# Performance work log

Hardware: AMD Instinct MI355X
Metric: run time of the kernel (lower is better)

## Reference

```python
import jax, jax.numpy as jnp
import numpy as np

TEMP = 0.1        # ds_temperature
THRESHOLD = 0.2
MARGIN = 2        # margin_remove


def setup_inputs() -> dict:
    key = jax.random.key(0)
    k0, k1 = jax.random.split(key)
    N, C = 2, 256
    h0, w0, h1, w1 = 60, 80, 60, 80
    feature0 = jax.random.normal(k0, (N, h0 * w0, C), dtype=jnp.float32)
    feature1 = jax.random.normal(k1, (N, h1 * w1, C), dtype=jnp.float32)
    return {"feature0": feature0, "feature1": feature1,
            "h0": h0, "w0": w0, "h1": h1, "w1": w1}


def _interior(n: int, b: int) -> jnp.ndarray:
    # True on [b, n-b), mirroring mask[:, :b]=False and mask[:, -b:]=False
    a = jnp.arange(n)
    return (a >= b) & (a < n - b)


def reference(feature0, feature1, h0, w0, h1, w1):
    N, L, C = feature0.shape
    S = feature1.shape[1]
    # similarities: (f0/sqrt(C)) . (f1/sqrt(C)) / temp == f0.f1 / (C*temp)
    sim = jnp.einsum('nlc,nsc->nls', feature0, feature1) / (C * TEMP)
    # dual softmax confidences
    conf = jax.nn.softmax(sim, axis=2) * jax.nn.softmax(sim, axis=1)
    # threshold mask with spatial margin removal (mask0 is None branch)
    mask = conf > THRESHOLD                      # [N, L, S]
    m5 = mask.reshape(N, h0, w0, h1, w1)
    valid = (_interior(h0, MARGIN)[:, None, None, None]
             & _interior(w0, MARGIN)[None, :, None, None]
             & _interior(h1, MARGIN)[None, None, :, None]
             & _interior(w1, MARGIN)[None, None, None, :])
    m5 = m5 & valid[None]
    mask = m5.reshape(N, L, S)
    # mutual nearest neighbor constraint
    mutual = ((conf == conf.max(axis=2, keepdims=True))
              & (conf == conf.max(axis=1, keepdims=True)))
    mask = mask & mutual
    # dense (jit-safe) encoding of the matches: confidences zeroed off-match.
    matched_conf = jnp.where(mask, conf, 0.0)
    return conf, mask, matched_conf
```

## Files before the change

kernel.cpp:

```cpp
#include <hip/hip_runtime.h>

#define NB 2
#define LD 4800
#define SD 4800
#define CD 256
#define H0 60
#define W0 80
#define H1 60
#define W1 80
#define MG 2
#define THRESH 0.2f
#define SIM_SCALE (1.0f / (256.0f * 0.1f))
#define GT 38
#define CAP 8192

typedef float f32x4 __attribute__((ext_vector_type(4)));
typedef __bf16 bf16x8 __attribute__((ext_vector_type(8)));
typedef unsigned short u16x8 __attribute__((ext_vector_type(8)));

#define GLOBAL_AS __attribute__((address_space(1)))
#define LDS_AS __attribute__((address_space(3)))

__device__ __forceinline__ void gl_lds16(const unsigned short* g, unsigned short* l) {
    __builtin_amdgcn_global_load_lds((const GLOBAL_AS unsigned int*)g,
                                     (LDS_AS unsigned int*)l, 16, 0, 0);
}

__device__ __forceinline__ unsigned short f2bf(float f) {
    unsigned int u = __float_as_uint(f);
    u = u + 0x7FFFu + ((u >> 16) & 1u);
    return (unsigned short)(u >> 16);
}

__device__ __forceinline__ bool interior0(int idx) {
    int i = idx / W0, j = idx % W0;
    return (i >= MG) & (i < H0 - MG) & (j >= MG) & (j < W0 - MG);
}
__device__ __forceinline__ bool interior1(int idx) {
    int i = idx / W1, j = idx % W1;
    return (i >= MG) & (i < H1 - MG) & (j >= MG) & (j < W1 - MG);
}

__global__ __launch_bounds__(256) void k_prep(float* __restrict__ p, int n) {
    int i = blockIdx.x * 256 + threadIdx.x;
    if (i < n) p[i] = 0.f;
}

__global__ __launch_bounds__(256) void k_cvt(const float* __restrict__ src,
                                             unsigned short* __restrict__ dst, int n8) {
    int i = blockIdx.x * 256 + threadIdx.x;
    if (i >= n8) return;
    const float4* s = (const float4*)src + (size_t)i * 2;
    float4 a = s[0], b = s[1];
    u16x8 o = {f2bf(a.x), f2bf(a.y), f2bf(a.z), f2bf(a.w),
               f2bf(b.x), f2bf(b.y), f2bf(b.z), f2bf(b.w)};
    *(u16x8*)(dst + (size_t)i * 8) = o;
}

template <int PASS>
__global__ __launch_bounds__(256) void k_gemm(const unsigned short* __restrict__ bA,
                                              const unsigned short* __restrict__ bB,
                                              float* __restrict__ rowsum,
                                              float* __restrict__ colsum,
                                              float* __restrict__ conf,
                                              float* __restrict__ mask,
                                              unsigned int* __restrict__ rowmax,
                                              unsigned int* __restrict__ colmax,
                                              unsigned int* __restrict__ cnt,
                                              uint4* __restrict__ list) {
    __shared__ __align__(16) unsigned short As[128][32];
    __shared__ __align__(16) unsigned short Bs[128][32];

    const int n  = blockIdx.z;
    const int s0 = blockIdx.x * 128;
    const int l0 = blockIdx.y * 128;
    const int tid  = threadIdx.x;
    const int lane = tid & 63;
    const int wave = tid >> 6;
    const int wm = (wave >> 1) * 64;
    const int wn = (wave & 1) * 64;
    const int quad = lane >> 4;
    const int lr   = lane & 15;

    const int sr = wave * 32 + (lane >> 2);
    const int sc = (lane & 3) * 8;
    const unsigned short* ga0 = bA + ((size_t)n * LD + min(l0 + sr,      LD - 1)) * CD + sc;
    const unsigned short* ga1 = bA + ((size_t)n * LD + min(l0 + sr + 16, LD - 1)) * CD + sc;
    const unsigned short* gb0 = bB + ((size_t)n * SD + min(s0 + sr,      SD - 1)) * CD + sc;
    const unsigned short* gb1 = bB + ((size_t)n * SD + min(s0 + sr + 16, SD - 1)) * CD + sc;
    unsigned short* la0 = &As[wave * 32][0];
    unsigned short* la1 = &As[wave * 32 + 16][0];
    unsigned short* lb0 = &Bs[wave * 32][0];
    unsigned short* lb1 = &Bs[wave * 32 + 16][0];

    f32x4 acc[4][4];
#pragma unroll
    for (int i = 0; i < 4; ++i)
#pragma unroll
        for (int j = 0; j < 4; ++j) acc[i][j] = (f32x4){0.f, 0.f, 0.f, 0.f};

    for (int k0 = 0; k0 < CD; k0 += 32) {
        __syncthreads();
        gl_lds16(ga0 + k0, la0);
        gl_lds16(ga1 + k0, la1);
        gl_lds16(gb0 + k0, lb0);
        gl_lds16(gb1 + k0, lb1);
        __syncthreads();

        bf16x8 af[4], bfr[4];
#pragma unroll
        for (int i = 0; i < 4; ++i) {
            af[i]  = __builtin_bit_cast(bf16x8, *(const u16x8*)&As[wm + i * 16 + lr][quad * 8]);
            bfr[i] = __builtin_bit_cast(bf16x8, *(const u16x8*)&Bs[wn + i * 16 + lr][quad * 8]);
        }
#pragma unroll
        for (int i = 0; i < 4; ++i)
#pragma unroll
            for (int j = 0; j < 4; ++j)
                acc[i][j] = __builtin_amdgcn_mfma_f32_16x16x32_bf16(af[i], bfr[j], acc[i][j], 0, 0, 0);
    }

    const int rb = l0 + wm;
    const int cb = s0 + wn;

    if (PASS == 0) {
        float rpart[4][4];
        float cpart[4];
#pragma unroll
        for (int i = 0; i < 4; ++i) {
            cpart[i] = 0.f;
#pragma unroll
            for (int g = 0; g < 4; ++g) rpart[i][g] = 0.f;
        }
#pragma unroll
        for (int mi = 0; mi < 4; ++mi)
#pragma unroll
            for (int ni = 0; ni < 4; ++ni)
#pragma unroll
                for (int g = 0; g < 4; ++g) {
                    int row = rb + mi * 16 + quad * 4 + g;
                    int col = cb + ni * 16 + lr;
                    float sv = acc[mi][ni][g] * SIM_SCALE;
                    bool ok = (row < LD) & (col < SD);
                    float ev = ok ? __expf(sv) : 0.f;
                    rpart[mi][g] += ev;
                    cpart[ni] += ev;
                }
#pragma unroll
        for (int mi = 0; mi < 4; ++mi)
#pragma unroll
            for (int g = 0; g < 4; ++g) {
                float v = rpart[mi][g];
                v += __shfl_xor(v, 1);
                v += __shfl_xor(v, 2);
                v += __shfl_xor(v, 4);
                v += __shfl_xor(v, 8);
                int row = rb + mi * 16 + quad * 4 + g;
                if (lr == 0 && row < LD) atomicAdd(&rowsum[n * LD + row], v);
            }
#pragma unroll
        for (int ni = 0; ni < 4; ++ni) {
            float v = cpart[ni];
            v += __shfl_xor(v, 16);
            v += __shfl_xor(v, 32);
            int col = cb + ni * 16 + lr;
            if (quad == 0 && col < SD) atomicAdd(&colsum[n * SD + col], v);
        }
    } else {
        {
            const size_t plane = (size_t)NB * LD * SD;
            f32x4* mask4  = (f32x4*)mask;
            f32x4* match4 = (f32x4*)(mask + plane);
            const int r0 = tid >> 5;
            const int c4 = tid & 31;
            const f32x4 z = {0.f, 0.f, 0.f, 0.f};
            if (s0 + c4 * 4 < SD) {
#pragma unroll
                for (int rr = 0; rr < 16; ++rr) {
                    int row = l0 + r0 + rr * 8;
                    if (row < LD) {
                        size_t o = ((size_t)n * LD + row) * (SD / 4) + (s0 / 4) + c4;
                        mask4[o]  = z;
                        match4[o] = z;
                    }
                }
            }
        }

        float rinv[4][4], cinv[4];
#pragma unroll
        for (int mi = 0; mi < 4; ++mi)
#pragma unroll
            for (int g = 0; g < 4; ++g) {
                int row = min(rb + mi * 16 + quad * 4 + g, LD - 1);
                rinv[mi][g] = rowsum[n * LD + row];
            }
#pragma unroll
        for (int ni = 0; ni < 4; ++ni) {
            int col = min(cb + ni * 16 + lr, SD - 1);
            cinv[ni] = colsum[n * SD + col];
        }
#pragma unroll
        for (int mi = 0; mi < 4; ++mi)
#pragma unroll
            for (int ni = 0; ni < 4; ++ni)
#pragma unroll
                for (int g = 0; g < 4; ++g) {
                    int row = rb + mi * 16 + quad * 4 + g;
                    int col = cb + ni * 16 + lr;
                    float sv = acc[mi][ni][g] * SIM_SCALE;
                    float e = __expf(sv);
                    float cv = e * e * rinv[mi][g] * cinv[ni];
                    bool ok = (row < LD) & (col < SD);
                    if (ok) {
                        conf[((size_t)n * LD + row) * SD + col] = cv;
                        if (cv > THRESH) {
                            atomicMax(&rowmax[n * LD + row], __float_as_uint(cv));
                            atomicMax(&colmax[n * SD + col], __float_as_uint(cv));
                            unsigned int id = atomicAdd(cnt, 1u);
                            if (id < CAP) {
                                uint4 rec = {(unsigned)n, (unsigned)row, (unsigned)col,
                                             __float_as_uint(cv)};
                                list[id] = rec;
                            }
                        }
                    }
                }
    }
}

__global__ __launch_bounds__(256) void k_inv(float* __restrict__ p, int n) {
    int i = blockIdx.x * 256 + threadIdx.x;
    if (i < n) p[i] = 1.0f / p[i];
}

__global__ __launch_bounds__(256) void k_fix(const unsigned int* __restrict__ cnt,
                                             const uint4* __restrict__ list,
                                             const unsigned int* __restrict__ rowmax,
                                             const unsigned int* __restrict__ colmax,
                                             float* __restrict__ mask,
                                             float* __restrict__ matched) {
    unsigned int m = min(*cnt, (unsigned int)CAP);
    for (unsigned int i = threadIdx.x; i < m; i += 256) {
        uint4 r = list[i];
        int n = (int)r.x, row = (int)r.y, col = (int)r.z;
        unsigned int cb = r.w;
        if (cb == rowmax[n * LD + row] && cb == colmax[n * SD + col] &&
            interior0(row) && interior1(col)) {
            size_t o = ((size_t)n * LD + row) * SD + col;
            mask[o] = 1.f;
            matched[o] = __uint_as_float(cb);
        }
    }
}

extern "C" void kernel_launch(void* const* d_in, const int* in_sizes, int n_in,
                              void* d_out, int out_size, void* d_ws, size_t ws_size,
                              hipStream_t stream) {
    const float* f0 = (const float*)d_in[0];
    const float* f1 = (const float*)d_in[1];
    const size_t plane = (size_t)NB * LD * SD;
    float* conf = (float*)d_out;
    float* mask = conf + plane;

    float* rowsum = (float*)d_ws;
    float* colsum = rowsum + NB * LD;
    unsigned int* rowmaxu = (unsigned int*)(colsum + NB * SD);
    unsigned int* colmaxu = rowmaxu + NB * LD;
    unsigned int* cnt = colmaxu + NB * SD;
    uint4* list = (uint4*)(cnt + 4);
    unsigned short* bf0 = (unsigned short*)(list + CAP);
    unsigned short* bf1 = bf0 + (size_t)NB * LD * CD;

    const int nz = NB * (LD + SD) * 2 + 4;
    k_prep<<<dim3((nz + 255) / 256), 256, 0, stream>>>(rowsum, nz);
    const int n8 = NB * LD * CD / 8;
    k_cvt<<<dim3((n8 + 255) / 256), 256, 0, stream>>>(f0, bf0, n8);
    k_cvt<<<dim3((n8 + 255) / 256), 256, 0, stream>>>(f1, bf1, n8);

    dim3 gg(GT, GT, NB);
    k_gemm<0><<<gg, 256, 0, stream>>>(bf0, bf1, rowsum, colsum, nullptr, nullptr,
                                      nullptr, nullptr, nullptr, nullptr);
    const int ninv = NB * (LD + SD);
    k_inv<<<dim3((ninv + 255) / 256), 256, 0, stream>>>(rowsum, ninv);
    k_gemm<1><<<gg, 256, 0, stream>>>(bf0, bf1, rowsum, colsum, conf, mask,
                                      rowmaxu, colmaxu, cnt, list);
    k_fix<<<dim3(1), 256, 0, stream>>>(cnt, list, rowmaxu, colmaxu, mask, mask + plane);
}
```

Baseline: 669.6 us.

## Stage conf epilogue through LDS for coalesced stores, double-buffer K loop, fuse prep kernels

The pass-1 epilogue now writes normalized confidences into an LDS buffer and stores them back as coalesced float4 rows, replacing scattered per-element global stores. The GEMM K loop is double-buffered so the next tile loads while the current one is multiplied. The zero-init and the two bf16 convert kernels are merged into one launch, and the reciprocal kernel is folded into the epilogue. This costs more LDS (a union of the tiles and a 64x132 float buffer) and an extra sync round per half-tile, which may lower occupancy.

```diff
diff --git a/kernel.cpp b/kernel.cpp
--- a/kernel.cpp
+++ b/kernel.cpp
@@ -41,21 +41,32 @@
     return (i >= MG) & (i < H1 - MG) & (j >= MG) & (j < W1 - MG);
 }
 
-__global__ __launch_bounds__(256) void k_prep(float* __restrict__ p, int n) {
-    int i = blockIdx.x * 256 + threadIdx.x;
-    if (i < n) p[i] = 0.f;
-}
-
-__global__ __launch_bounds__(256) void k_cvt(const float* __restrict__ src,
-                                             unsigned short* __restrict__ dst, int n8) {
-    int i = blockIdx.x * 256 + threadIdx.x;
-    if (i >= n8) return;
-    const float4* s = (const float4*)src + (size_t)i * 2;
-    float4 a = s[0], b = s[1];
-    u16x8 o = {f2bf(a.x), f2bf(a.y), f2bf(a.z), f2bf(a.w),
-               f2bf(b.x), f2bf(b.y), f2bf(b.z), f2bf(b.w)};
-    *(u16x8*)(dst + (size_t)i * 8) = o;
-}
+__global__ __launch_bounds__(256) void k_init(const float* __restrict__ f0,
+                                              const float* __restrict__ f1,
+                                              unsigned short* __restrict__ bf0,
+                                              unsigned short* __restrict__ bf1,
+                                              float* __restrict__ stats, int nstat) {
+    const int per = NB * LD * CD / 8;
+    int t = blockIdx.x * 256 + threadIdx.x;
+    if (t < 2 * per) {
+        const float* src;
+        unsigned short* dst;
+        int i;
+        if (t < per) { src = f0; dst = bf0; i = t; }
+        else         { src = f1; dst = bf1; i = t - per; }
+        const float4* s = (const float4*)src + (size_t)i * 2;
+        float4 a = s[0], b = s[1];
+        u16x8 o = {f2bf(a.x), f2bf(a.y), f2bf(a.z), f2bf(a.w),
+                   f2bf(b.x), f2bf(b.y), f2bf(b.z), f2bf(b.w)};
+        *(u16x8*)(dst + (size_t)i * 8) = o;
+    }
+    if (t < nstat) stats[t] = 0.f;
+}
+
+union SMem {
+    struct { unsigned short As[2][128][32]; unsigned short Bs[2][128][32]; } g;
+    float cbuf[64][132];
+};
 
 template <int PASS>
 __global__ __launch_bounds__(256) void k_gemm(const unsigned short* __restrict__ bA,
@@ -68,8 +79,7 @@
                                               unsigned int* __restrict__ colmax,
                                               unsigned int* __restrict__ cnt,
                                               uint4* __restrict__ list) {
-    __shared__ __align__(16) unsigned short As[128][32];
-    __shared__ __align__(16) unsigned short Bs[128][32];
+    __shared__ __align__(16) SMem sm;
 
     const int n  = blockIdx.z;
     const int s0 = blockIdx.x * 128;
@@ -88,10 +98,6 @@
     const unsigned short* ga1 = bA + ((size_t)n * LD + min(l0 + sr + 16, LD - 1)) * CD + sc;
     const unsigned short* gb0 = bB + ((size_t)n * SD + min(s0 + sr,      SD - 1)) * CD + sc;
     const unsigned short* gb1 = bB + ((size_t)n * SD + min(s0 + sr + 16, SD - 1)) * CD + sc;
-    unsigned short* la0 = &As[wave * 32][0];
-    unsigned short* la1 = &As[wave * 32 + 16][0];
-    unsigned short* lb0 = &Bs[wave * 32][0];
-    unsigned short* lb1 = &Bs[wave * 32 + 16][0];
 
     f32x4 acc[4][4];
 #pragma unroll
@@ -99,19 +105,27 @@
 #pragma unroll
         for (int j = 0; j < 4; ++j) acc[i][j] = (f32x4){0.f, 0.f, 0.f, 0.f};
 
-    for (int k0 = 0; k0 < CD; k0 += 32) {
+    gl_lds16(ga0, &sm.g.As[0][wave * 32][0]);
+    gl_lds16(ga1, &sm.g.As[0][wave * 32 + 16][0]);
+    gl_lds16(gb0, &sm.g.Bs[0][wave * 32][0]);
+    gl_lds16(gb1, &sm.g.Bs[0][wave * 32 + 16][0]);
+
+#pragma unroll
+    for (int t = 0; t < 8; ++t) {
+        const int cur = t & 1;
         __syncthreads();
-        gl_lds16(ga0 + k0, la0);
-        gl_lds16(ga1 + k0, la1);
-        gl_lds16(gb0 + k0, lb0);
-        gl_lds16(gb1 + k0, lb1);
-        __syncthreads();
-
+        if (t < 7) {
+            const int k0 = (t + 1) * 32;
+            gl_lds16(ga0 + k0, &sm.g.As[cur ^ 1][wave * 32][0]);
+            gl_lds16(ga1 + k0, &sm.g.As[cur ^ 1][wave * 32 + 16][0]);
+            gl_lds16(gb0 + k0, &sm.g.Bs[cur ^ 1][wave * 32][0]);
+            gl_lds16(gb1 + k0, &sm.g.Bs[cur ^ 1][wave * 32 + 16][0]);
+        }
         bf16x8 af[4], bfr[4];
 #pragma unroll
         for (int i = 0; i < 4; ++i) {
-            af[i]  = __builtin_bit_cast(bf16x8, *(const u16x8*)&As[wm + i * 16 + lr][quad * 8]);
-            bfr[i] = __builtin_bit_cast(bf16x8, *(const u16x8*)&Bs[wn + i * 16 + lr][quad * 8]);
+            af[i]  = __builtin_bit_cast(bf16x8, *(const u16x8*)&sm.g.As[cur][wm + i * 16 + lr][quad * 8]);
+            bfr[i] = __builtin_bit_cast(bf16x8, *(const u16x8*)&sm.g.Bs[cur][wn + i * 16 + lr][quad * 8]);
         }
 #pragma unroll
         for (int i = 0; i < 4; ++i)
@@ -167,6 +181,71 @@
             if (quad == 0 && col < SD) atomicAdd(&colsum[n * SD + col], v);
         }
     } else {
+        float rinv[4][4], cinv[4];
+#pragma unroll
+        for (int mi = 0; mi < 4; ++mi)
+#pragma unroll
+            for (int g = 0; g < 4; ++g) {
+                int row = min(rb + mi * 16 + quad * 4 + g, LD - 1);
+                rinv[mi][g] = 1.0f / rowsum[n * LD + row];
+            }
+#pragma unroll
+        for (int ni = 0; ni < 4; ++ni) {
+            int col = min(cb + ni * 16 + lr, SD - 1);
+            cinv[ni] = 1.0f / colsum[n * SD + col];
+        }
+
+        const size_t rowpitch4 = SD / 4;
+#pragma unroll
+        for (int h = 0; h < 2; ++h) {
+            __syncthreads();
+            if ((wm >> 6) == h) {
+#pragma unroll
+                for (int mi = 0; mi < 4; ++mi)
+#pragma unroll
+                    for (int ni = 0; ni < 4; ++ni)
+#pragma unroll
+                        for (int g = 0; g < 4; ++g) {
+                            int r = mi * 16 + quad * 4 + g;
+                            int c = wn + ni * 16 + lr;
+                            float sv = acc[mi][ni][g] * SIM_SCALE;
+                            float e = __expf(sv);
+                            sm.cbuf[r][c] = e * e * rinv[mi][g] * cinv[ni];
+                        }
+            }
+            __syncthreads();
+            const int r0 = tid >> 5;
+            const int c4 = tid & 31;
+            const int col0 = s0 + c4 * 4;
+#pragma unroll
+            for (int j = 0; j < 8; ++j) {
+                int r = r0 + j * 8;
+                int row = l0 + h * 64 + r;
+                if ((row < LD) & (col0 < SD)) {
+                    f32x4 v = *(const f32x4*)&sm.cbuf[r][c4 * 4];
+                    *(f32x4*)(conf + ((size_t)n * LD + row) * SD + col0) = v;
+                    if (v[0] > THRESH || v[1] > THRESH || v[2] > THRESH || v[3] > THRESH) {
+#pragma unroll
+                        for (int e4 = 0; e4 < 4; ++e4) {
+                            float cv = v[e4];
+                            if (cv > THRESH) {
+                                int col = col0 + e4;
+                                unsigned int vb = __float_as_uint(cv);
+                                atomicMax(&rowmax[n * LD + row], vb);
+                                atomicMax(&colmax[n * SD + col], vb);
+                                unsigned int id = atomicAdd(cnt, 1u);
+                                if (id < CAP) {
+                                    uint4 rec = {(unsigned)n, (unsigned)row,
+                                                 (unsigned)col, vb};
+                                    list[id] = rec;
+                                }
+                            }
+                        }
+                    }
+                }
+            }
+        }
+
         {
             const size_t plane = (size_t)NB * LD * SD;
             f32x4* mask4  = (f32x4*)mask;
@@ -179,59 +258,14 @@
                 for (int rr = 0; rr < 16; ++rr) {
                     int row = l0 + r0 + rr * 8;
                     if (row < LD) {
-                        size_t o = ((size_t)n * LD + row) * (SD / 4) + (s0 / 4) + c4;
+                        size_t o = ((size_t)n * LD + row) * rowpitch4 + (s0 / 4) + c4;
                         mask4[o]  = z;
                         match4[o] = z;
                     }
                 }
             }
         }
-
-        float rinv[4][4], cinv[4];
-#pragma unroll
-        for (int mi = 0; mi < 4; ++mi)
-#pragma unroll
-            for (int g = 0; g < 4; ++g) {
-                int row = min(rb + mi * 16 + quad * 4 + g, LD - 1);
-                rinv[mi][g] = rowsum[n * LD + row];
-            }
-#pragma unroll
-        for (int ni = 0; ni < 4; ++ni) {
-            int col = min(cb + ni * 16 + lr, SD - 1);
-            cinv[ni] = colsum[n * SD + col];
-        }
-#pragma unroll
-        for (int mi = 0; mi < 4; ++mi)
-#pragma unroll
-            for (int ni = 0; ni < 4; ++ni)
-#pragma unroll
-                for (int g = 0; g < 4; ++g) {
-                    int row = rb + mi * 16 + quad * 4 + g;
-                    int col = cb + ni * 16 + lr;
-                    float sv = acc[mi][ni][g] * SIM_SCALE;
-                    float e = __expf(sv);
-                    float cv = e * e * rinv[mi][g] * cinv[ni];
-                    bool ok = (row < LD) & (col < SD);
-                    if (ok) {
-                        conf[((size_t)n * LD + row) * SD + col] = cv;
-                        if (cv > THRESH) {
-                            atomicMax(&rowmax[n * LD + row], __float_as_uint(cv));
-                            atomicMax(&colmax[n * SD + col], __float_as_uint(cv));
-                            unsigned int id = atomicAdd(cnt, 1u);
-                            if (id < CAP) {
-                                uint4 rec = {(unsigned)n, (unsigned)row, (unsigned)col,
-                                             __float_as_uint(cv)};
-                                list[id] = rec;
-                            }
-                        }
-                    }
-                }
     }
-}
-
-__global__ __launch_bounds__(256) void k_inv(float* __restrict__ p, int n) {
-    int i = blockIdx.x * 256 + threadIdx.x;
-    if (i < n) p[i] = 1.0f / p[i];
 }
 
 __global__ __launch_bounds__(256) void k_fix(const unsigned int* __restrict__ cnt,
@@ -272,17 +306,13 @@
     unsigned short* bf0 = (unsigned short*)(list + CAP);
     unsigned short* bf1 = bf0 + (size_t)NB * LD * CD;
 
-    const int nz = NB * (LD + SD) * 2 + 4;
-    k_prep<<<dim3((nz + 255) / 256), 256, 0, stream>>>(rowsum, nz);
-    const int n8 = NB * LD * CD / 8;
-    k_cvt<<<dim3((n8 + 255) / 256), 256, 0, stream>>>(f0, bf0, n8);
-    k_cvt<<<dim3((n8 + 255) / 256), 256, 0, stream>>>(f1, bf1, n8);
+    const int nstat = NB * (LD + SD) * 2 + 4;
+    k_init<<<dim3(2 * NB * LD * CD / 8 / 256), 256, 0, stream>>>(f0, f1, bf0, bf1,
+                                                                 rowsum, nstat);
 
     dim3 gg(GT, GT, NB);
     k_gemm<0><<<gg, 256, 0, stream>>>(bf0, bf1, rowsum, colsum, nullptr, nullptr,
                                       nullptr, nullptr, nullptr, nullptr);
-    const int ninv = NB * (LD + SD);
-    k_inv<<<dim3((ninv + 255) / 256), 256, 0, stream>>>(rowsum, ninv);
     k_gemm<1><<<gg, 256, 0, stream>>>(bf0, bf1, rowsum, colsum, conf, mask,
                                       rowmaxu, colmaxu, cnt, list);
     k_fix<<<dim3(1), 256, 0, stream>>>(cnt, list, rowmaxu, colmaxu, mask, mask + plane);
```

After: 688.3 us. 1.03x slower.
